# Optimization experiments

Hardware: AMD Instinct MI355X
Metric: run time of the kernel (lower is better)

## Reference

```python
import jax, jax.numpy as jnp
import numpy as np

HIDDEN = 1024
SCALE = float(np.sqrt(HIDDEN))  # canonical sqrt(d) scale factor


def setup_inputs() -> dict:
    key = jax.random.key(0)
    ks = jax.random.split(key, 10)
    B, S, D = 4, 2048, HIDDEN
    bound = 1.0 / np.sqrt(D)  # torch Linear default init range
    inp = {
        "q": jax.random.normal(ks[0], (B, S, D), dtype=jnp.float32),
        "k": jax.random.normal(ks[1], (B, S, D), dtype=jnp.float32),
        "v": jax.random.normal(ks[2], (B, S, D), dtype=jnp.float32),
        "mask": jnp.zeros((B, S, S), dtype=bool),  # unused by original forward
        "Wq": jax.random.uniform(ks[3], (D, D), jnp.float32, -bound, bound),
        "bq": jax.random.uniform(ks[4], (D,), jnp.float32, -bound, bound),
        "Wk": jax.random.uniform(ks[5], (D, D), jnp.float32, -bound, bound),
        "bk": jax.random.uniform(ks[6], (D,), jnp.float32, -bound, bound),
        "Wv": jax.random.uniform(ks[7], (D, D), jnp.float32, -bound, bound),
        "bv": jax.random.uniform(ks[8], (D,), jnp.float32, -bound, bound),
    }
    return inp


def reference(q, k, v, mask, Wq, bq, Wk, bk, Wv, bv):
    # torch Linear: y = x @ W.T + b
    qp = jnp.einsum("bsd,ed->bse", q, Wq) + bq  # [B,S,D]
    kp = jnp.einsum("bsd,ed->bse", k, Wk) + bk
    vp = jnp.einsum("bsd,ed->bse", v, Wv) + bv
    scores = jnp.einsum("bqd,bkd->bqk", qp, kp) / SCALE  # [B,S,S]
    attn = jax.nn.softmax(scores, axis=-1)
    # dropout with p=0 (dropout_p undefined in source) -> identity
    out = jnp.einsum("bqk,bkd->bqd", attn, vp)  # [B,S,D]
    return out
```

## Files before the change

### kernel.cpp

```cpp
#include <hip/hip_runtime.h>

#define S_ 2048
#define D_ 1024
#define MTOT 8192

typedef __attribute__((ext_vector_type(8))) short bf16x8;
typedef __attribute__((ext_vector_type(8))) unsigned short ush8;
typedef __attribute__((ext_vector_type(4))) float f32x4;

__device__ __forceinline__ unsigned short f2bf(float x) {
    unsigned u = __builtin_bit_cast(unsigned, x);
    u += 0x7fffu + ((u >> 16) & 1u);
    return (unsigned short)(u >> 16);
}

__device__ __forceinline__ void async16(const unsigned short* g, unsigned short* l) {
    __builtin_amdgcn_global_load_lds(
        (const __attribute__((address_space(1))) unsigned int*)(g),
        (__attribute__((address_space(3))) unsigned int*)(l),
        16, 0, 0);
}

__global__ __launch_bounds__(256)
void tobf16_kernel(const float* __restrict__ s0, const float* __restrict__ s1,
                   const float* __restrict__ s2, const float* __restrict__ s3,
                   const float* __restrict__ s4, const float* __restrict__ s5,
                   unsigned short* __restrict__ d0, unsigned short* __restrict__ d1,
                   unsigned short* __restrict__ d2, unsigned short* __restrict__ d3,
                   unsigned short* __restrict__ d4, unsigned short* __restrict__ d5)
{
    const float* src; unsigned short* dst; size_t n;
    switch (blockIdx.y) {
        case 0: src = s0; dst = d0; n = (size_t)MTOT * D_; break;
        case 1: src = s1; dst = d1; n = (size_t)MTOT * D_; break;
        case 2: src = s2; dst = d2; n = (size_t)MTOT * D_; break;
        case 3: src = s3; dst = d3; n = (size_t)D_ * D_;   break;
        case 4: src = s4; dst = d4; n = (size_t)D_ * D_;   break;
        default: src = s5; dst = d5; n = (size_t)D_ * D_;  break;
    }
    size_t base = ((size_t)blockIdx.x * 256 + threadIdx.x) * 8;
    if (base >= n) return;
    float4 a = *reinterpret_cast<const float4*>(src + base);
    float4 b = *reinterpret_cast<const float4*>(src + base + 4);
    ush8 h;
    h[0] = f2bf(a.x); h[1] = f2bf(a.y); h[2] = f2bf(a.z); h[3] = f2bf(a.w);
    h[4] = f2bf(b.x); h[5] = f2bf(b.y); h[6] = f2bf(b.z); h[7] = f2bf(b.w);
    *reinterpret_cast<ush8*>(dst + base) = h;
}

template<int EPI>
__global__ __launch_bounds__(256)
void gemm_nt(const unsigned short* __restrict__ Ag, const unsigned short* __restrict__ Bg,
             const float* __restrict__ bias, float* __restrict__ Cf,
             unsigned short* __restrict__ Cbf,
             int K, float alpha, int ldc, size_t sA, size_t sB, size_t sC)
{
    __shared__ unsigned short As[128 * 32];
    __shared__ unsigned short Bs[128 * 32];
    const int zb = blockIdx.z;
    Ag += (size_t)zb * sA;
    Bg += (size_t)zb * sB;

    const int t = threadIdx.x;
    const int w = t >> 6, lane = t & 63;
    const int m0 = blockIdx.x * 128, n0 = blockIdx.y * 128;
    const int wm = (w >> 1) * 64, wn = (w & 1) * 64;
    const int lr = lane & 15, lk4 = lane >> 4;

    const int c0 = (w * 2 + 0) * 64 + lane;
    const int c1 = (w * 2 + 1) * 64 + lane;
    const unsigned short* ga0 = Ag + (size_t)(m0 + (c0 >> 2)) * K + (c0 & 3) * 8;
    const unsigned short* ga1 = Ag + (size_t)(m0 + (c1 >> 2)) * K + (c1 & 3) * 8;
    const unsigned short* gb0 = Bg + (size_t)(n0 + (c0 >> 2)) * K + (c0 & 3) * 8;
    const unsigned short* gb1 = Bg + (size_t)(n0 + (c1 >> 2)) * K + (c1 & 3) * 8;
    unsigned short* la0 = As + (w * 2 + 0) * 512;
    unsigned short* la1 = As + (w * 2 + 1) * 512;
    unsigned short* lb0 = Bs + (w * 2 + 0) * 512;
    unsigned short* lb1 = Bs + (w * 2 + 1) * 512;

    f32x4 acc[4][4];
    const f32x4 z4 = {0.f, 0.f, 0.f, 0.f};
    for (int i = 0; i < 4; i++) for (int j = 0; j < 4; j++) acc[i][j] = z4;

    for (int k0 = 0; k0 < K; k0 += 32) {
        __syncthreads();
        async16(ga0, la0); async16(ga1, la1);
        async16(gb0, lb0); async16(gb1, lb1);
        ga0 += 32; ga1 += 32; gb0 += 32; gb1 += 32;
        __syncthreads();
        bf16x8 af[4], bfr[4];
        for (int mi = 0; mi < 4; mi++)
            af[mi] = *reinterpret_cast<const bf16x8*>(As + (wm + mi * 16 + lr) * 32 + lk4 * 8);
        for (int ni = 0; ni < 4; ni++)
            bfr[ni] = *reinterpret_cast<const bf16x8*>(Bs + (wn + ni * 16 + lr) * 32 + lk4 * 8);
        for (int mi = 0; mi < 4; mi++)
            for (int ni = 0; ni < 4; ni++)
                acc[mi][ni] = __builtin_amdgcn_mfma_f32_16x16x32_bf16(af[mi], bfr[ni], acc[mi][ni], 0, 0, 0);
    }

    for (int mi = 0; mi < 4; mi++) {
        const int mbase = m0 + wm + mi * 16 + lk4 * 4;
        for (int ni = 0; ni < 4; ni++) {
            const int nn = n0 + wn + ni * 16 + lr;
            float bb = (EPI >= 1) ? bias[nn] : 0.f;
            for (int r = 0; r < 4; r++) {
                const int m = mbase + r;
                float val = acc[mi][ni][r];
                if (EPI == 0) {
                    Cf[(size_t)zb * sC + (size_t)m * ldc + nn] = alpha * val;
                } else if (EPI == 1) {
                    Cbf[(size_t)m * ldc + nn] = f2bf(val + bb);
                } else {
                    const int batch = m >> 11, ss = m & 2047;
                    Cbf[((size_t)(batch << 10) + nn) * S_ + ss] = f2bf(val + bb);
                }
            }
        }
    }
}

__global__ __launch_bounds__(256)
void softmax_kernel(const float* __restrict__ s, unsigned short* __restrict__ P)
{
    const size_t row = blockIdx.x;
    const int t = threadIdx.x;
    const float* sp = s + row * 2048 + (size_t)t * 8;
    float4 a = *reinterpret_cast<const float4*>(sp);
    float4 b = *reinterpret_cast<const float4*>(sp + 4);
    float x[8] = {a.x, a.y, a.z, a.w, b.x, b.y, b.z, b.w};

    float m = x[0];
    for (int j = 1; j < 8; j++) m = fmaxf(m, x[j]);
    for (int off = 1; off < 64; off <<= 1) m = fmaxf(m, __shfl_xor(m, off));
    __shared__ float redm[4], reds[4];
    const int w = t >> 6;
    if ((t & 63) == 0) redm[w] = m;
    __syncthreads();
    m = fmaxf(fmaxf(redm[0], redm[1]), fmaxf(redm[2], redm[3]));

    float e[8]; float sum = 0.f;
    for (int j = 0; j < 8; j++) { e[j] = __expf(x[j] - m); sum += e[j]; }
    for (int off = 1; off < 64; off <<= 1) sum += __shfl_xor(sum, off);
    if ((t & 63) == 0) reds[w] = sum;
    __syncthreads();
    sum = reds[0] + reds[1] + reds[2] + reds[3];
    const float inv = 1.0f / sum;

    ush8 h;
    for (int j = 0; j < 8; j++) h[j] = f2bf(e[j] * inv);
    *reinterpret_cast<ush8*>(P + row * 2048 + (size_t)t * 8) = h;
}

extern "C" void kernel_launch(void* const* d_in, const int* in_sizes, int n_in,
                              void* d_out, int out_size, void* d_ws, size_t ws_size,
                              hipStream_t stream)
{
    const float* q  = (const float*)d_in[0];
    const float* k  = (const float*)d_in[1];
    const float* v  = (const float*)d_in[2];
    const float* Wq = (const float*)d_in[4];
    const float* bq = (const float*)d_in[5];
    const float* Wk = (const float*)d_in[6];
    const float* bk = (const float*)d_in[7];
    const float* Wv = (const float*)d_in[8];
    const float* bv = (const float*)d_in[9];
    float* out = (float*)d_out;

    const size_t MB = (size_t)1 << 20;
    const size_t need = 198 * MB;
    if (ws_size < need) return;
    char* ws = (char*)d_ws;
    unsigned short* qbf  = (unsigned short*)(ws + 0 * MB);
    unsigned short* kbf  = (unsigned short*)(ws + 16 * MB);
    unsigned short* vbf  = (unsigned short*)(ws + 32 * MB);
    unsigned short* wqbf = (unsigned short*)(ws + 48 * MB);
    unsigned short* wkbf = (unsigned short*)(ws + 50 * MB);
    unsigned short* wvbf = (unsigned short*)(ws + 52 * MB);
    unsigned short* qp   = (unsigned short*)(ws + 54 * MB);
    unsigned short* kp   = (unsigned short*)(ws + 70 * MB);
    unsigned short* vT   = (unsigned short*)(ws + 86 * MB);
    float*          sc   = (float*)         (ws + 102 * MB);
    unsigned short* P    = (unsigned short*)(ws + 166 * MB);

    dim3 blk(256);

    tobf16_kernel<<<dim3(4096, 6), blk, 0, stream>>>(q, k, v, Wq, Wk, Wv,
                                                     qbf, kbf, vbf, wqbf, wkbf, wvbf);

    gemm_nt<1><<<dim3(64, 8), blk, 0, stream>>>(qbf, wqbf, bq, nullptr, qp,
                                                D_, 1.f, D_, 0, 0, 0);
    gemm_nt<1><<<dim3(64, 8), blk, 0, stream>>>(kbf, wkbf, bk, nullptr, kp,
                                                D_, 1.f, D_, 0, 0, 0);
    gemm_nt<2><<<dim3(64, 8), blk, 0, stream>>>(vbf, wvbf, bv, nullptr, vT,
                                                D_, 1.f, D_, 0, 0, 0);

    gemm_nt<0><<<dim3(16, 16, 4), blk, 0, stream>>>(qp, kp, nullptr, sc, nullptr,
                                                    D_, 0.03125f, S_,
                                                    (size_t)S_ * D_, (size_t)S_ * D_, (size_t)S_ * S_);

    softmax_kernel<<<dim3(MTOT), blk, 0, stream>>>(sc, P);

    gemm_nt<0><<<dim3(16, 8, 4), blk, 0, stream>>>(P, vT, nullptr, out, nullptr,
                                                   S_, 1.f, D_,
                                                   (size_t)S_ * S_, (size_t)D_ * S_, (size_t)S_ * D_);
}
```

Measured before the change: 257.3 us.

## Double-buffer GEMM LDS tiles, swizzle LDS layout, remap blocks across XCDs, vectorize transpose store

The GEMM now uses two LDS buffers, so the async global-to-LDS loads for the next K-step are issued before the MFMAs on the current step. This replaces the two barriers per iteration with one. The LDS column chunk is XOR-swizzled on both write and read to reduce bank conflicts. Workgroup IDs are remapped so consecutive tiles land on the same XCD for better L2 reuse, and the transposed V epilogue writes four bf16 values at once instead of scalar stores. The cost is doubled LDS use, which may lower occupancy, plus extra index arithmetic.

```diff
diff --git a/kernel.cpp b/kernel.cpp
--- a/kernel.cpp
+++ b/kernel.cpp
@@ -6,6 +6,7 @@
 
 typedef __attribute__((ext_vector_type(8))) short bf16x8;
 typedef __attribute__((ext_vector_type(8))) unsigned short ush8;
+typedef __attribute__((ext_vector_type(4))) unsigned short ush4;
 typedef __attribute__((ext_vector_type(4))) float f32x4;
 
 __device__ __forceinline__ unsigned short f2bf(float x) {
@@ -19,6 +20,10 @@
         (const __attribute__((address_space(1))) unsigned int*)(g),
         (__attribute__((address_space(3))) unsigned int*)(l),
         16, 0, 0);
+}
+
+__device__ __forceinline__ int xcd_remap(int id, int nwg) {
+    return (id & 7) * (nwg >> 3) + (id >> 3);
 }
 
 __global__ __launch_bounds__(256)
@@ -55,44 +60,71 @@
              unsigned short* __restrict__ Cbf,
              int K, float alpha, int ldc, size_t sA, size_t sB, size_t sC)
 {
-    __shared__ unsigned short As[128 * 32];
-    __shared__ unsigned short Bs[128 * 32];
-    const int zb = blockIdx.z;
-    Ag += (size_t)zb * sA;
-    Bg += (size_t)zb * sB;
+    __shared__ unsigned short As[2][128 * 32];
+    __shared__ unsigned short Bs[2][128 * 32];
+
+    const int gx = gridDim.x, gy = gridDim.y;
+    const int nwg = gx * gy * gridDim.z;
+    int id = xcd_remap(blockIdx.x + gx * (blockIdx.y + gy * blockIdx.z), nwg);
+    const int bx = id % gx; id /= gx;
+    const int by = id % gy;
+    const int bz = id / gy;
+
+    Ag += (size_t)bz * sA;
+    Bg += (size_t)bz * sB;
 
     const int t = threadIdx.x;
     const int w = t >> 6, lane = t & 63;
-    const int m0 = blockIdx.x * 128, n0 = blockIdx.y * 128;
+    const int m0 = bx * 128, n0 = by * 128;
     const int wm = (w >> 1) * 64, wn = (w & 1) * 64;
     const int lr = lane & 15, lk4 = lane >> 4;
 
-    const int c0 = (w * 2 + 0) * 64 + lane;
-    const int c1 = (w * 2 + 1) * 64 + lane;
-    const unsigned short* ga0 = Ag + (size_t)(m0 + (c0 >> 2)) * K + (c0 & 3) * 8;
-    const unsigned short* ga1 = Ag + (size_t)(m0 + (c1 >> 2)) * K + (c1 & 3) * 8;
-    const unsigned short* gb0 = Bg + (size_t)(n0 + (c0 >> 2)) * K + (c0 & 3) * 8;
-    const unsigned short* gb1 = Bg + (size_t)(n0 + (c1 >> 2)) * K + (c1 & 3) * 8;
-    unsigned short* la0 = As + (w * 2 + 0) * 512;
-    unsigned short* la1 = As + (w * 2 + 1) * 512;
-    unsigned short* lb0 = Bs + (w * 2 + 0) * 512;
-    unsigned short* lb1 = Bs + (w * 2 + 1) * 512;
+    const int s0i = w * 2, s1i = w * 2 + 1;
+    const int r0 = s0i * 16 + (lane >> 2);
+    const int r1 = s1i * 16 + (lane >> 2);
+    const int jsrc = ((lane & 3) ^ ((lane >> 3) & 3)) * 8;
+    const unsigned short* ga0 = Ag + (size_t)(m0 + r0) * K + jsrc;
+    const unsigned short* ga1 = Ag + (size_t)(m0 + r1) * K + jsrc;
+    const unsigned short* gb0 = Bg + (size_t)(n0 + r0) * K + jsrc;
+    const unsigned short* gb1 = Bg + (size_t)(n0 + r1) * K + jsrc;
+
+    const int krd = (lk4 ^ ((lr >> 1) & 3)) * 8;
 
     f32x4 acc[4][4];
     const f32x4 z4 = {0.f, 0.f, 0.f, 0.f};
     for (int i = 0; i < 4; i++) for (int j = 0; j < 4; j++) acc[i][j] = z4;
 
-    for (int k0 = 0; k0 < K; k0 += 32) {
+    async16(ga0, &As[0][s0i * 512]); async16(ga1, &As[0][s1i * 512]);
+    async16(gb0, &Bs[0][s0i * 512]); async16(gb1, &Bs[0][s1i * 512]);
+    ga0 += 32; ga1 += 32; gb0 += 32; gb1 += 32;
+    __syncthreads();
+
+    int cur = 0;
+    const int nsteps = K >> 5;
+    for (int step = 1; step < nsteps; ++step) {
+        const int nxt = cur ^ 1;
+        async16(ga0, &As[nxt][s0i * 512]); async16(ga1, &As[nxt][s1i * 512]);
+        async16(gb0, &Bs[nxt][s0i * 512]); async16(gb1, &Bs[nxt][s1i * 512]);
+        ga0 += 32; ga1 += 32; gb0 += 32; gb1 += 32;
+
+        bf16x8 af[4], bfr[4];
+        for (int mi = 0; mi < 4; mi++)
+            af[mi] = *reinterpret_cast<const bf16x8*>(&As[cur][(wm + mi * 16 + lr) * 32 + krd]);
+        for (int ni = 0; ni < 4; ni++)
+            bfr[ni] = *reinterpret_cast<const bf16x8*>(&Bs[cur][(wn + ni * 16 + lr) * 32 + krd]);
+        for (int mi = 0; mi < 4; mi++)
+            for (int ni = 0; ni < 4; ni++)
+                acc[mi][ni] = __builtin_amdgcn_mfma_f32_16x16x32_bf16(af[mi], bfr[ni], acc[mi][ni], 0, 0, 0);
+
         __syncthreads();
-        async16(ga0, la0); async16(ga1, la1);
-        async16(gb0, lb0); async16(gb1, lb1);
-        ga0 += 32; ga1 += 32; gb0 += 32; gb1 += 32;
-        __syncthreads();
+        cur = nxt;
+    }
+    {
         bf16x8 af[4], bfr[4];
         for (int mi = 0; mi < 4; mi++)
-            af[mi] = *reinterpret_cast<const bf16x8*>(As + (wm + mi * 16 + lr) * 32 + lk4 * 8);
+            af[mi] = *reinterpret_cast<const bf16x8*>(&As[cur][(wm + mi * 16 + lr) * 32 + krd]);
         for (int ni = 0; ni < 4; ni++)
-            bfr[ni] = *reinterpret_cast<const bf16x8*>(Bs + (wn + ni * 16 + lr) * 32 + lk4 * 8);
+            bfr[ni] = *reinterpret_cast<const bf16x8*>(&Bs[cur][(wn + ni * 16 + lr) * 32 + krd]);
         for (int mi = 0; mi < 4; mi++)
             for (int ni = 0; ni < 4; ni++)
                 acc[mi][ni] = __builtin_amdgcn_mfma_f32_16x16x32_bf16(af[mi], bfr[ni], acc[mi][ni], 0, 0, 0);
@@ -103,16 +135,19 @@
         for (int ni = 0; ni < 4; ni++) {
             const int nn = n0 + wn + ni * 16 + lr;
             float bb = (EPI >= 1) ? bias[nn] : 0.f;
-            for (int r = 0; r < 4; r++) {
-                const int m = mbase + r;
-                float val = acc[mi][ni][r];
-                if (EPI == 0) {
-                    Cf[(size_t)zb * sC + (size_t)m * ldc + nn] = alpha * val;
-                } else if (EPI == 1) {
-                    Cbf[(size_t)m * ldc + nn] = f2bf(val + bb);
-                } else {
-                    const int batch = m >> 11, ss = m & 2047;
-                    Cbf[((size_t)(batch << 10) + nn) * S_ + ss] = f2bf(val + bb);
+            if (EPI == 2) {
+                const int batch = mbase >> 11, ss = mbase & 2047;
+                ush4 hv;
+                for (int r = 0; r < 4; r++) hv[r] = f2bf(acc[mi][ni][r] + bb);
+                *reinterpret_cast<ush4*>(Cbf + ((size_t)(batch << 10) + nn) * S_ + ss) = hv;
+            } else {
+                for (int r = 0; r < 4; r++) {
+                    const int m = mbase + r;
+                    float val = acc[mi][ni][r];
+                    if (EPI == 0)
+                        Cf[(size_t)bz * sC + (size_t)m * ldc + nn] = alpha * val;
+                    else
+                        Cbf[(size_t)m * ldc + nn] = f2bf(val + bb);
                 }
             }
         }
```

Result: no change. 255.2 us (-0.8%).

## Replace GEMMs with 256-tile double-buffered pipelined kernels, merge projections, XCD remap

Applied to the files above, without the earlier changes.

Replaces the 128x128, K=32 single-buffered GEMM with a 256x256 (or 128x256) tile, K=64 kernel using 512 threads. It double-buffers LDS with async global-to-LDS loads, XOR-swizzles LDS to avoid bank conflicts, and uses explicit waitcnt, barriers and setprio to overlap loads with MFMA. The three projection GEMMs are merged into one launch, and workgroup IDs are remapped across XCDs for cache locality. The V-transpose epilogue now writes vectorized 4-element stores. The large LDS footprint (64KB per block for the 256 tiles) and register pressure could limit occupancy.

```diff
diff --git a/kernel.cpp b/kernel.cpp
--- a/kernel.cpp
+++ b/kernel.cpp
@@ -6,6 +6,7 @@
 
 typedef __attribute__((ext_vector_type(8))) short bf16x8;
 typedef __attribute__((ext_vector_type(8))) unsigned short ush8;
+typedef __attribute__((ext_vector_type(4))) unsigned short ush4;
 typedef __attribute__((ext_vector_type(4))) float f32x4;
 
 __device__ __forceinline__ unsigned short f2bf(float x) {
@@ -19,6 +20,19 @@
         (const __attribute__((address_space(1))) unsigned int*)(g),
         (__attribute__((address_space(3))) unsigned int*)(l),
         16, 0, 0);
+}
+
+#define FENCE() asm volatile("" ::: "memory")
+#define SBAR()  __builtin_amdgcn_s_barrier()
+#define SCHED0() __builtin_amdgcn_sched_barrier(0)
+
+template<int N> __device__ __forceinline__ void waitv();
+template<> __device__ __forceinline__ void waitv<0>() { asm volatile("s_waitcnt vmcnt(0)" ::: "memory"); }
+template<> __device__ __forceinline__ void waitv<2>() { asm volatile("s_waitcnt vmcnt(2)" ::: "memory"); }
+template<> __device__ __forceinline__ void waitv<4>() { asm volatile("s_waitcnt vmcnt(4)" ::: "memory"); }
+
+__device__ __forceinline__ int xcd_remap(int id, int nwg) {
+    return (id & 7) * (nwg >> 3) + (id >> 3);
 }
 
 __global__ __launch_bounds__(256)
@@ -48,75 +62,200 @@
     *reinterpret_cast<ush8*>(dst + base) = h;
 }
 
-template<int EPI>
-__global__ __launch_bounds__(256)
-void gemm_nt(const unsigned short* __restrict__ Ag, const unsigned short* __restrict__ Bg,
-             const float* __restrict__ bias, float* __restrict__ Cf,
-             unsigned short* __restrict__ Cbf,
-             int K, float alpha, int ldc, size_t sA, size_t sB, size_t sC)
-{
-    __shared__ unsigned short As[128 * 32];
-    __shared__ unsigned short Bs[128 * 32];
-    const int zb = blockIdx.z;
-    Ag += (size_t)zb * sA;
-    Bg += (size_t)zb * sB;
+template<int EPI, int BM>
+__device__ __forceinline__ void gemm_body(
+    unsigned short* As, unsigned short* Bs,
+    const unsigned short* __restrict__ Ag, const unsigned short* __restrict__ Bg,
+    const float* __restrict__ bias,
+    float* __restrict__ Cf, unsigned short* __restrict__ Cbf,
+    int K, float alpha, int ldc, int m0, int n0, size_t coff)
+{
+    constexpr int WM    = BM / 2;
+    constexpr int MI    = WM / 16;
+    constexpr int MIH   = MI / 2;
+    constexpr int ASLAB = BM / 64;
+    constexpr int ABUF  = BM * 64;
+    constexpr int BBUF  = 256 * 64;
 
     const int t = threadIdx.x;
     const int w = t >> 6, lane = t & 63;
-    const int m0 = blockIdx.x * 128, n0 = blockIdx.y * 128;
-    const int wm = (w >> 1) * 64, wn = (w & 1) * 64;
+    const int wr = w >> 2, wc = w & 3;
     const int lr = lane & 15, lk4 = lane >> 4;
 
-    const int c0 = (w * 2 + 0) * 64 + lane;
-    const int c1 = (w * 2 + 1) * 64 + lane;
-    const unsigned short* ga0 = Ag + (size_t)(m0 + (c0 >> 2)) * K + (c0 & 3) * 8;
-    const unsigned short* ga1 = Ag + (size_t)(m0 + (c1 >> 2)) * K + (c1 & 3) * 8;
-    const unsigned short* gb0 = Bg + (size_t)(n0 + (c0 >> 2)) * K + (c0 & 3) * 8;
-    const unsigned short* gb1 = Bg + (size_t)(n0 + (c1 >> 2)) * K + (c1 & 3) * 8;
-    unsigned short* la0 = As + (w * 2 + 0) * 512;
-    unsigned short* la1 = As + (w * 2 + 1) * 512;
-    unsigned short* lb0 = Bs + (w * 2 + 0) * 512;
-    unsigned short* lb1 = Bs + (w * 2 + 1) * 512;
-
-    f32x4 acc[4][4];
+    const int crow = t >> 3;
+    const int cj   = ((t & 7) ^ ((t >> 4) & 3)) * 8;
+
+    auto stA = [&](int buf, int s, int kt) {
+        async16(Ag + (size_t)(m0 + s * 64 + crow) * K + kt * 64 + cj,
+                As + buf * ABUF + s * 4096 + w * 512);
+    };
+    auto stB = [&](int buf, int s, int kt) {
+        async16(Bg + (size_t)(n0 + s * 64 + crow) * K + kt * 64 + cj,
+                Bs + buf * BBUF + s * 4096 + w * 512);
+    };
+    auto rdA = [&](int buf, int rr, int kk) -> bf16x8 {
+        const int phys = ((kk * 4 + lk4) ^ ((rr >> 1) & 3)) * 8;
+        return *reinterpret_cast<const bf16x8*>(As + buf * ABUF + rr * 64 + phys);
+    };
+    auto rdB = [&](int buf, int rr, int kk) -> bf16x8 {
+        const int phys = ((kk * 4 + lk4) ^ ((rr >> 1) & 3)) * 8;
+        return *reinterpret_cast<const bf16x8*>(Bs + buf * BBUF + rr * 64 + phys);
+    };
+
+    f32x4 acc[MI][4];
     const f32x4 z4 = {0.f, 0.f, 0.f, 0.f};
-    for (int i = 0; i < 4; i++) for (int j = 0; j < 4; j++) acc[i][j] = z4;
-
-    for (int k0 = 0; k0 < K; k0 += 32) {
-        __syncthreads();
-        async16(ga0, la0); async16(ga1, la1);
-        async16(gb0, lb0); async16(gb1, lb1);
-        ga0 += 32; ga1 += 32; gb0 += 32; gb1 += 32;
-        __syncthreads();
-        bf16x8 af[4], bfr[4];
-        for (int mi = 0; mi < 4; mi++)
-            af[mi] = *reinterpret_cast<const bf16x8*>(As + (wm + mi * 16 + lr) * 32 + lk4 * 8);
-        for (int ni = 0; ni < 4; ni++)
-            bfr[ni] = *reinterpret_cast<const bf16x8*>(Bs + (wn + ni * 16 + lr) * 32 + lk4 * 8);
-        for (int mi = 0; mi < 4; mi++)
-            for (int ni = 0; ni < 4; ni++)
-                acc[mi][ni] = __builtin_amdgcn_mfma_f32_16x16x32_bf16(af[mi], bfr[ni], acc[mi][ni], 0, 0, 0);
+#pragma unroll
+    for (int i = 0; i < MI; i++)
+#pragma unroll
+        for (int j = 0; j < 4; j++) acc[i][j] = z4;
+
+    const int NT = K >> 6;
+
+#pragma unroll
+    for (int s = 0; s < ASLAB; ++s) stA(0, s, 0);
+#pragma unroll
+    for (int s = 0; s < 4; ++s)     stB(0, s, 0);
+#pragma unroll
+    for (int s = 0; s < ASLAB; ++s) stA(1, s, 1);
+    waitv<ASLAB>(); SCHED0(); SBAR(); FENCE();
+
+    for (int kt = 0; kt < NT; ++kt) {
+        const int cur = kt & 1;
+        if (kt + 1 < NT) {
+#pragma unroll
+            for (int s = 0; s < 4; ++s) stB(cur ^ 1, s, kt + 1);
+        }
+
+        bf16x8 bfr[4][2];
+#pragma unroll
+        for (int ni = 0; ni < 4; ++ni)
+#pragma unroll
+            for (int kk = 0; kk < 2; ++kk)
+                bfr[ni][kk] = rdB(cur, wc * 64 + ni * 16 + lr, kk);
+
+        bf16x8 af[MIH][2];
+#pragma unroll
+        for (int mi = 0; mi < MIH; ++mi)
+#pragma unroll
+            for (int kk = 0; kk < 2; ++kk)
+                af[mi][kk] = rdA(cur, wr * WM + mi * 16 + lr, kk);
+        __builtin_amdgcn_s_setprio(1);
+#pragma unroll
+        for (int mi = 0; mi < MIH; ++mi)
+#pragma unroll
+            for (int ni = 0; ni < 4; ++ni)
+#pragma unroll
+                for (int kk = 0; kk < 2; ++kk)
+                    acc[mi][ni] = __builtin_amdgcn_mfma_f32_16x16x32_bf16(af[mi][kk], bfr[ni][kk], acc[mi][ni], 0, 0, 0);
+        __builtin_amdgcn_s_setprio(0);
+
+#pragma unroll
+        for (int mi = 0; mi < MIH; ++mi)
+#pragma unroll
+            for (int kk = 0; kk < 2; ++kk)
+                af[mi][kk] = rdA(cur, wr * WM + (MIH + mi) * 16 + lr, kk);
+        __builtin_amdgcn_s_setprio(1);
+#pragma unroll
+        for (int mi = 0; mi < MIH; ++mi)
+#pragma unroll
+            for (int ni = 0; ni < 4; ++ni)
+#pragma unroll
+                for (int kk = 0; kk < 2; ++kk)
+                    acc[MIH + mi][ni] = __builtin_amdgcn_mfma_f32_16x16x32_bf16(af[mi][kk], bfr[ni][kk], acc[MIH + mi][ni], 0, 0, 0);
+        __builtin_amdgcn_s_setprio(0);
+
+        FENCE(); SBAR();
+        if (kt + 2 < NT) {
+#pragma unroll
+            for (int s = 0; s < ASLAB; ++s) stA(cur, s, kt + 2);
+            waitv<ASLAB>();
+        } else if (kt + 1 < NT) {
+            waitv<0>();
+        }
+        if (kt + 1 < NT) { SCHED0(); SBAR(); FENCE(); }
     }
 
-    for (int mi = 0; mi < 4; mi++) {
-        const int mbase = m0 + wm + mi * 16 + lk4 * 4;
-        for (int ni = 0; ni < 4; ni++) {
-            const int nn = n0 + wn + ni * 16 + lr;
-            float bb = (EPI >= 1) ? bias[nn] : 0.f;
-            for (int r = 0; r < 4; r++) {
-                const int m = mbase + r;
-                float val = acc[mi][ni][r];
-                if (EPI == 0) {
-                    Cf[(size_t)zb * sC + (size_t)m * ldc + nn] = alpha * val;
-                } else if (EPI == 1) {
-                    Cbf[(size_t)m * ldc + nn] = f2bf(val + bb);
-                } else {
-                    const int batch = m >> 11, ss = m & 2047;
-                    Cbf[((size_t)(batch << 10) + nn) * S_ + ss] = f2bf(val + bb);
-                }
+#pragma unroll
+    for (int mi = 0; mi < MI; ++mi) {
+        const int mbase = m0 + wr * WM + mi * 16 + lk4 * 4;
+#pragma unroll
+        for (int ni = 0; ni < 4; ++ni) {
+            const int nn = n0 + wc * 64 + ni * 16 + lr;
+            if constexpr (EPI == 0) {
+#pragma unroll
+                for (int r = 0; r < 4; ++r)
+                    Cf[coff + (size_t)(mbase + r) * ldc + nn] = alpha * acc[mi][ni][r];
+            } else if constexpr (EPI == 1) {
+                const float bb = bias[nn];
+#pragma unroll
+                for (int r = 0; r < 4; ++r)
+                    Cbf[(size_t)(mbase + r) * ldc + nn] = f2bf(acc[mi][ni][r] + bb);
+            } else {
+                const float bb = bias[nn];
+                const int batch = mbase >> 11, ss = mbase & 2047;
+                ush4 hv;
+#pragma unroll
+                for (int r = 0; r < 4; ++r) hv[r] = f2bf(acc[mi][ni][r] + bb);
+                *reinterpret_cast<ush4*>(Cbf + ((size_t)(batch << 10) + nn) * S_ + ss) = hv;
             }
         }
     }
+}
+
+__global__ __launch_bounds__(512, 2)
+void proj256(const unsigned short* __restrict__ q, const unsigned short* __restrict__ k,
+             const unsigned short* __restrict__ v,
+             const unsigned short* __restrict__ wq, const unsigned short* __restrict__ wk,
+             const unsigned short* __restrict__ wv,
+             const float* __restrict__ bq, const float* __restrict__ bk,
+             const float* __restrict__ bv,
+             unsigned short* __restrict__ qp, unsigned short* __restrict__ kp,
+             unsigned short* __restrict__ vT)
+{
+    __shared__ unsigned short As[2 * 256 * 64];
+    __shared__ unsigned short Bs[2 * 256 * 64];
+    int id = xcd_remap(blockIdx.x + 32 * (blockIdx.y + 4 * blockIdx.z), 32 * 4 * 3);
+    const int bx = id % 32; id /= 32;
+    const int by = id % 4;
+    const int bz = id / 4;
+    const unsigned short *A, *Bm; const float* bb; unsigned short* Ob;
+    if (bz == 0)      { A = q; Bm = wq; bb = bq; Ob = qp; }
+    else if (bz == 1) { A = k; Bm = wk; bb = bk; Ob = kp; }
+    else              { A = v; Bm = wv; bb = bv; Ob = vT; }
+    if (bz == 2)
+        gemm_body<2, 256>(As, Bs, A, Bm, bb, nullptr, Ob, D_, 1.f, D_, bx * 256, by * 256, 0);
+    else
+        gemm_body<1, 256>(As, Bs, A, Bm, bb, nullptr, Ob, D_, 1.f, D_, bx * 256, by * 256, 0);
+}
+
+__global__ __launch_bounds__(512, 2)
+void qk256(const unsigned short* __restrict__ qp, const unsigned short* __restrict__ kp,
+           float* __restrict__ sc)
+{
+    __shared__ unsigned short As[2 * 256 * 64];
+    __shared__ unsigned short Bs[2 * 256 * 64];
+    int id = xcd_remap(blockIdx.x + 8 * (blockIdx.y + 8 * blockIdx.z), 8 * 8 * 4);
+    const int bx = id % 8; id /= 8;
+    const int by = id % 8;
+    const int bz = id / 8;
+    gemm_body<0, 256>(As, Bs, qp + (size_t)bz * S_ * D_, kp + (size_t)bz * S_ * D_,
+                      nullptr, sc, nullptr, D_, 0.03125f, S_,
+                      bx * 256, by * 256, (size_t)bz * S_ * S_);
+}
+
+__global__ __launch_bounds__(512, 2)
+void pv128(const unsigned short* __restrict__ P, const unsigned short* __restrict__ vT,
+           float* __restrict__ out)
+{
+    __shared__ unsigned short As[2 * 128 * 64];
+    __shared__ unsigned short Bs[2 * 256 * 64];
+    int id = xcd_remap(blockIdx.x + 16 * (blockIdx.y + 4 * blockIdx.z), 16 * 4 * 4);
+    const int bx = id % 16; id /= 16;
+    const int by = id % 4;
+    const int bz = id / 4;
+    gemm_body<0, 128>(As, Bs, P + (size_t)bz * S_ * S_, vT + (size_t)bz * D_ * S_,
+                      nullptr, out, nullptr, S_, 1.f, D_,
+                      bx * 128, by * 256, (size_t)bz * S_ * D_);
 }
 
 __global__ __launch_bounds__(256)
@@ -182,25 +321,15 @@
     float*          sc   = (float*)         (ws + 102 * MB);
     unsigned short* P    = (unsigned short*)(ws + 166 * MB);
 
-    dim3 blk(256);
-
-    tobf16_kernel<<<dim3(4096, 6), blk, 0, stream>>>(q, k, v, Wq, Wk, Wv,
-                                                     qbf, kbf, vbf, wqbf, wkbf, wvbf);
-
-    gemm_nt<1><<<dim3(64, 8), blk, 0, stream>>>(qbf, wqbf, bq, nullptr, qp,
-                                                D_, 1.f, D_, 0, 0, 0);
-    gemm_nt<1><<<dim3(64, 8), blk, 0, stream>>>(kbf, wkbf, bk, nullptr, kp,
-                                                D_, 1.f, D_, 0, 0, 0);
-    gemm_nt<2><<<dim3(64, 8), blk, 0, stream>>>(vbf, wvbf, bv, nullptr, vT,
-                                                D_, 1.f, D_, 0, 0, 0);
-
-    gemm_nt<0><<<dim3(16, 16, 4), blk, 0, stream>>>(qp, kp, nullptr, sc, nullptr,
-                                                    D_, 0.03125f, S_,
-                                                    (size_t)S_ * D_, (size_t)S_ * D_, (size_t)S_ * S_);
-
-    softmax_kernel<<<dim3(MTOT), blk, 0, stream>>>(sc, P);
-
-    gemm_nt<0><<<dim3(16, 8, 4), blk, 0, stream>>>(P, vT, nullptr, out, nullptr,
-                                                   S_, 1.f, D_,
-                                                   (size_t)S_ * S_, (size_t)D_ * S_, (size_t)S_ * D_);
-}
+    tobf16_kernel<<<dim3(4096, 6), dim3(256), 0, stream>>>(q, k, v, Wq, Wk, Wv,
+                                                           qbf, kbf, vbf, wqbf, wkbf, wvbf);
+
+    proj256<<<dim3(32, 4, 3), dim3(512), 0, stream>>>(qbf, kbf, vbf, wqbf, wkbf, wvbf,
+                                                      bq, bk, bv, qp, kp, vT);
+
+    qk256<<<dim3(8, 8, 4), dim3(512), 0, stream>>>(qp, kp, sc);
+
+    softmax_kernel<<<dim3(MTOT), dim3(256), 0, stream>>>(sc, P);
+
+    pv128<<<dim3(16, 4, 4), dim3(512), 0, stream>>>(P, vT, out);
+}
```

Measured after the change: 233.2 us. -9.4%, faster.
